# Kernel optimization log

Measured on AMD Instinct MI355X. Metric: run time of the kernel, lower is better.

The kernel has to match this reference:

```python
import jax, jax.numpy as jnp
import numpy as np
import math

D_MODEL = 1024
N_HEADS = 16
D_HEAD = D_MODEL // N_HEADS
DECAY_MAX = 0.99  # buggy torch init: only the LAST head's decay rate survives the loop
LN_EPS = 1e-5


def setup_inputs() -> dict:
    key = jax.random.key(0)
    ks = jax.random.split(key, 12)
    B, S = 2, 2048
    x = jax.random.normal(ks[0], (B, S, D_MODEL), dtype=jnp.float32)
    def w(k):
        return jax.random.normal(k, (D_MODEL, D_MODEL), dtype=jnp.float32) * 0.02
    return {
        "x": x,
        "Wq": w(ks[1]), "bq": jnp.zeros((D_MODEL,), jnp.float32),
        "Wk": w(ks[2]), "bk": jnp.zeros((D_MODEL,), jnp.float32),
        "Wv": w(ks[3]), "bv": jnp.zeros((D_MODEL,), jnp.float32),
        "Wg": w(ks[4]), "bg": jnp.zeros((D_MODEL,), jnp.float32),
        "Wo": w(ks[5]), "bo": jnp.zeros((D_MODEL,), jnp.float32),
        "gamma": jnp.ones((D_MODEL,), jnp.float32),
        "beta": jnp.zeros((D_MODEL,), jnp.float32),
    }


def _decay_mask(S):
    # faithful to torch buffer: decay_matrix[i,j] = DECAY_MAX**(i-j) for j<=i else 0
    i = jnp.arange(S, dtype=jnp.float32)[:, None]
    j = jnp.arange(S, dtype=jnp.float32)[None, :]
    diff = i - j
    return jnp.where(diff >= 0, jnp.power(jnp.float32(DECAY_MAX), diff), 0.0)  # [S,S]


def reference(x, Wq, bq, Wk, bk, Wv, bv, Wg, bg, Wo, bo, gamma, beta):
    B, S, D = x.shape
    H, DH = N_HEADS, D_HEAD
    # projections -> [B,H,S,DH]
    Q = (x @ Wq + bq).reshape(B, S, H, DH).transpose(0, 2, 1, 3)
    K = (x @ Wk + bk).reshape(B, S, H, DH).transpose(0, 2, 1, 3)
    V = (x @ Wv + bv).reshape(B, S, H, DH).transpose(0, 2, 1, 3)
    scores = jnp.einsum('bhsd,bhtd->bhst', Q, K) / math.sqrt(DH)  # [B,H,S,S]
    mask = _decay_mask(S)  # [S,S], broadcast over B,H (head-independent per torch bug)
    retained = jnp.einsum('bhst,bhtd->bhsd', scores * mask, V)
    retained = retained.transpose(0, 2, 1, 3).reshape(B, S, D)
    # LayerNorm over last dim
    mu = jnp.mean(retained, axis=-1, keepdims=True)
    var = jnp.var(retained, axis=-1, keepdims=True)
    normed = (retained - mu) * jax.lax.rsqrt(var + LN_EPS) * gamma + beta
    G = jax.nn.sigmoid(x @ Wg + bg)
    return (normed * G) @ Wo + bo  # dropout = identity (eval)
```

## Files before the change

### kernel.cpp

```cpp
#include <hip/hip_runtime.h>

typedef __attribute__((ext_vector_type(4))) float f32x4;
typedef __attribute__((ext_vector_type(8))) short bf16x8;
typedef unsigned short USHORT;

static __device__ __forceinline__ float bf2f(USHORT u) {
    return __uint_as_float(((unsigned)u) << 16);
}
static __device__ __forceinline__ USHORT f2bf(float f) {
    unsigned u = __float_as_uint(f);
    unsigned r = u + 0x7FFF + ((u >> 16) & 1);
    return (USHORT)(r >> 16);
}

#define GLDS16(gp, lp) __builtin_amdgcn_global_load_lds(                      \
    (const __attribute__((address_space(1))) unsigned int*)(gp),              \
    (__attribute__((address_space(3))) unsigned int*)(lp), 16, 0, 0)

#define FULL_BARRIER() asm volatile("s_waitcnt vmcnt(0) lgkmcnt(0)\ns_barrier" ::: "memory")

#define D64 0.52559648f
#define L2D (-0.014499569695115089f)

struct PrepArgs { const float* src[5]; USHORT* dst[5]; const float* x; USHORT* xb; };

__global__ __launch_bounds__(256) void k_prep(PrepArgs pa) {
    const int z = blockIdx.z;
    const int tid = threadIdx.x;
    __shared__ USHORT t[64][65];
    if (z < 5) {
        const float* __restrict__ W  = pa.src[z];
        USHORT* __restrict__      WT = pa.dst[z];
        const int k0 = blockIdx.y * 64, n0 = blockIdx.x * 64;
#pragma unroll
        for (int s = 0; s < 4; s++) {
            int slot = tid + s * 256;
            int row = slot >> 4, c4 = (slot & 15) * 4;
            float4 vv = *(const float4*)&W[(size_t)(k0 + row) * 1024 + n0 + c4];
            t[row][c4 + 0] = f2bf(vv.x);
            t[row][c4 + 1] = f2bf(vv.y);
            t[row][c4 + 2] = f2bf(vv.z);
            t[row][c4 + 3] = f2bf(vv.w);
        }
        __syncthreads();
#pragma unroll
        for (int s = 0; s < 2; s++) {
            int slot = tid + s * 256;
            int n = slot >> 3, c8 = (slot & 7) * 8;
            USHORT tmp[8];
#pragma unroll
            for (int u = 0; u < 8; u++) tmp[u] = t[c8 + u][n];
            *(int4*)&WT[(size_t)(n0 + n) * 1024 + k0 + c8] = *(int4*)tmp;
        }
    } else {
        const int bi = blockIdx.y * 16 + blockIdx.x;
        const float* xs = pa.x + (size_t)bi * 16384;
        USHORT* xd = pa.xb + (size_t)bi * 16384;
#pragma unroll
        for (int u = 0; u < 16; u++) {
            int idx = u * 1024 + tid * 4;
            float4 v = *(const float4*)&xs[idx];
            *(ushort4*)&xd[idx] = make_ushort4(f2bf(v.x), f2bf(v.y), f2bf(v.z), f2bf(v.w));
        }
    }
}

struct GArgs {
    const USHORT* A;
    const USHORT* W[4];
    const float*  bias[4];
    void*         dst[4];
    USHORT*       dstv;
    float         scale[4];
    int           mode[4];
};

__global__ __launch_bounds__(256, 2) void k_gemm(GArgs ga) {
    const int z = blockIdx.z;
    const USHORT* __restrict__ A  = ga.A;
    const USHORT* __restrict__ BT = ga.W[z];
    __shared__ USHORT As[2][128 * 32];
    __shared__ USHORT Bs[2][128 * 32];
    const int tid = threadIdx.x;
    const int m0 = blockIdx.y * 128, n0 = blockIdx.x * 128;
    const int w = tid >> 6, l = tid & 63, lr = l & 15, q = l >> 4;
    const int wr = w >> 1, wc = w & 1;
    const int srow = tid >> 2, sco = (tid & 3) * 8;
    f32x4 acc[4][4] = {};
    GLDS16(&A [(size_t)(m0 + srow)      * 1024 + sco], &As[0][srow * 32 + sco]);
    GLDS16(&A [(size_t)(m0 + srow + 64) * 1024 + sco], &As[0][(srow + 64) * 32 + sco]);
    GLDS16(&BT[(size_t)(n0 + srow)      * 1024 + sco], &Bs[0][srow * 32 + sco]);
    GLDS16(&BT[(size_t)(n0 + srow + 64) * 1024 + sco], &Bs[0][(srow + 64) * 32 + sco]);
    for (int kt = 0; kt < 32; kt++) {
        const int cur = kt & 1;
        FULL_BARRIER();
        if (kt + 1 < 32) {
            const int k1 = (kt + 1) * 32;
            const int nxt = 1 - cur;
            GLDS16(&A [(size_t)(m0 + srow)      * 1024 + k1 + sco], &As[nxt][srow * 32 + sco]);
            GLDS16(&A [(size_t)(m0 + srow + 64) * 1024 + k1 + sco], &As[nxt][(srow + 64) * 32 + sco]);
            GLDS16(&BT[(size_t)(n0 + srow)      * 1024 + k1 + sco], &Bs[nxt][srow * 32 + sco]);
            GLDS16(&BT[(size_t)(n0 + srow + 64) * 1024 + k1 + sco], &Bs[nxt][(srow + 64) * 32 + sco]);
        }
        bf16x8 af[4], bfr[4];
#pragma unroll
        for (int mi = 0; mi < 4; mi++)
            af[mi] = *(const bf16x8*)&As[cur][(wr * 64 + mi * 16 + lr) * 32 + q * 8];
#pragma unroll
        for (int ni = 0; ni < 4; ni++)
            bfr[ni] = *(const bf16x8*)&Bs[cur][(wc * 64 + ni * 16 + lr) * 32 + q * 8];
#pragma unroll
        for (int mi = 0; mi < 4; mi++)
#pragma unroll
            for (int ni = 0; ni < 4; ni++)
                acc[mi][ni] = __builtin_amdgcn_mfma_f32_16x16x32_bf16(
                    af[mi], bfr[ni], acc[mi][ni], 0, 0, 0);
    }
    const float scale = ga.scale[z];
    const int mode = ga.mode[z];
    const float* __restrict__ bias = ga.bias[z];
#pragma unroll
    for (int ni = 0; ni < 4; ni++) {
        int col = n0 + wc * 64 + ni * 16 + lr;
        float bv = bias[col];
#pragma unroll
        for (int mi = 0; mi < 4; mi++) {
            int r0 = m0 + wr * 64 + mi * 16 + q * 4;
            float vr[4];
#pragma unroll
            for (int r = 0; r < 4; r++) {
                float v = acc[mi][ni][r] + bv;
                if (mode == 1) v = 1.0f / (1.0f + __expf(-v));
                vr[r] = v * scale;
            }
            if (mode == 3) {
                float* df = (float*)ga.dst[z];
#pragma unroll
                for (int r = 0; r < 4; r++)
                    df[(size_t)(r0 + r) * 1024 + col] = vr[r];
            } else if (mode == 2) {
                int b = r0 >> 11, s = r0 & 2047;
                int h = col >> 6, d = col & 63;
                const float NP1 = 1.0101010101010102f;
                float c0 = exp2f(-L2D * (float)(s & 63));
                float c1 = c0 * NP1, c2 = c1 * NP1, c3 = c2 * NP1;
                *(ushort4*)&ga.dstv[(size_t)(((b * 16 + h) * 64) + d) * 2048 + s] =
                    make_ushort4(f2bf(vr[0] * c0), f2bf(vr[1] * c1),
                                 f2bf(vr[2] * c2), f2bf(vr[3] * c3));
            } else {
                USHORT* db = (USHORT*)ga.dst[z];
#pragma unroll
                for (int r = 0; r < 4; r++)
                    db[(size_t)(r0 + r) * 1024 + col] = f2bf(vr[r]);
            }
        }
    }
}

__global__ __launch_bounds__(256) void k_attn_u(const USHORT* __restrict__ K,
                                                const USHORT* __restrict__ VT,
                                                float* __restrict__ U) {
    const int bh = blockIdx.x, c = blockIdx.y;
    const int b = bh >> 4, h = bh & 15;
    const int tid = threadIdx.x, w = tid >> 6, l = tid & 63, lr = l & 15, q = l >> 4;
    __shared__ USHORT KT[64 * 72];
    __shared__ USHORT Vs[64 * 72];
#pragma unroll
    for (int s = 0; s < 2; s++) {
        int slot = tid + s * 256;
        int row = slot >> 3, co = (slot & 7) * 8;
        USHORT kv[8];
        *(int4*)kv = *(const int4*)&K[(size_t)(b * 2048 + c * 64 + row) * 1024 + h * 64 + co];
#pragma unroll
        for (int u = 0; u < 8; u++) KT[(co + u) * 72 + row] = kv[u];
        *(int4*)&Vs[row * 72 + co] =
            *(const int4*)&VT[(size_t)(bh * 64 + row) * 2048 + c * 64 + co];
    }
    __syncthreads();
    f32x4 acc[4] = {};
    bf16x8 av[2];
#pragma unroll
    for (int kk = 0; kk < 2; kk++)
        av[kk] = *(const bf16x8*)&Vs[(w * 16 + lr) * 72 + kk * 32 + q * 8];
#pragma unroll
    for (int dkt = 0; dkt < 4; dkt++)
#pragma unroll
        for (int kk = 0; kk < 2; kk++) {
            bf16x8 bk = *(const bf16x8*)&KT[(dkt * 16 + lr) * 72 + kk * 32 + q * 8];
            acc[dkt] = __builtin_amdgcn_mfma_f32_16x16x32_bf16(av[kk], bk, acc[dkt], 0, 0, 0);
        }
    float* slot = U + (size_t)(bh * 32 + c) * 4096;
#pragma unroll
    for (int dkt = 0; dkt < 4; dkt++)
#pragma unroll
        for (int r = 0; r < 4; r++)
            slot[(w * 16 + q * 4 + r) * 64 + dkt * 16 + lr] = acc[dkt][r] * D64;
}

__global__ __launch_bounds__(256, 2) void k_apply(const USHORT* __restrict__ Q,
                                                  const USHORT* __restrict__ K,
                                                  const USHORT* __restrict__ VT,
                                                  const float* __restrict__ U,
                                                  USHORT* __restrict__ R,
                                                  float* __restrict__ stats) {
    const int bh = blockIdx.x, c = blockIdx.y;
    const int b = bh >> 4, h = bh & 15;
    const int i0 = c * 64;
    const int tid = threadIdx.x, w = tid >> 6, l = tid & 63, lr = l & 15, q = l >> 4;
    __shared__ USHORT Qs[64 * 72];
    __shared__ USHORT Ks[64 * 72];
    __shared__ USHORT Vs[64 * 72];
    __shared__ USHORT Ps[4][16 * 72];
    __shared__ unsigned Spk[4096];
#pragma unroll
    for (int s = 0; s < 2; s++) {
        int slot = tid + s * 256;
        int row = slot >> 3, c8 = (slot & 7) * 8;
        USHORT q8[8];
        *(int4*)q8 = *(const int4*)&Q[(size_t)(b * 2048 + i0 + row) * 1024 + h * 64 + c8];
        const float fr = exp2f(L2D * (float)row);
#pragma unroll
        for (int u = 0; u < 8; u++) q8[u] = f2bf(bf2f(q8[u]) * fr);
        *(int4*)&Qs[row * 72 + c8] = *(int4*)q8;
        *(int4*)&Ks[row * 72 + c8] =
            *(const int4*)&K[(size_t)(b * 2048 + i0 + row) * 1024 + h * 64 + c8];
        *(int4*)&Vs[row * 72 + c8] =
            *(const int4*)&VT[(size_t)(bh * 64 + row) * 2048 + i0 + c8];
    }
    if (c > 0) {
        float sa[16] = {};
        const float* Ub = U + (size_t)bh * 32 * 4096 + tid * 16;
        for (int cp = 0; cp < c; cp++) {
            const float* p = Ub + (size_t)cp * 4096;
#pragma unroll
            for (int u4 = 0; u4 < 4; u4++) {
                float4 uv = *(const float4*)(p + u4 * 4);
                sa[u4 * 4 + 0] = sa[u4 * 4 + 0] * D64 + uv.x;
                sa[u4 * 4 + 1] = sa[u4 * 4 + 1] * D64 + uv.y;
                sa[u4 * 4 + 2] = sa[u4 * 4 + 2] * D64 + uv.z;
                sa[u4 * 4 + 3] = sa[u4 * 4 + 3] * D64 + uv.w;
            }
        }
#pragma unroll
        for (int u = 0; u < 16; u++) {
            USHORT hi = f2bf(sa[u]);
            float  lo = sa[u] - bf2f(hi);
            Spk[tid * 16 + u] = (unsigned)hi | ((unsigned)f2bf(lo) << 16);
        }
    }
    __syncthreads();
    bf16x8 bqf[2];
#pragma unroll
    for (int kk = 0; kk < 2; kk++)
        bqf[kk] = *(const bf16x8*)&Qs[(w * 16 + lr) * 72 + kk * 32 + q * 8];
    f32x4 accr[4] = {};
    if (c > 0) {
#pragma unroll
        for (int dt = 0; dt < 4; dt++)
#pragma unroll
            for (int kk = 0; kk < 2; kk++) {
                const unsigned* sp = &Spk[(dt * 16 + lr) * 64 + kk * 32 + q * 8];
                uint4 pa = *(const uint4*)sp;
                uint4 pb = *(const uint4*)(sp + 4);
                unsigned pk[8] = { pa.x, pa.y, pa.z, pa.w, pb.x, pb.y, pb.z, pb.w };
                bf16x8 hi, lo;
#pragma unroll
                for (int u = 0; u < 8; u++) {
                    hi[u] = (short)(pk[u] & 0xffffu);
                    lo[u] = (short)(pk[u] >> 16);
                }
                accr[dt] = __builtin_amdgcn_mfma_f32_16x16x32_bf16(hi, bqf[kk], accr[dt], 0, 0, 0);
                accr[dt] = __builtin_amdgcn_mfma_f32_16x16x32_bf16(lo, bqf[kk], accr[dt], 0, 0, 0);
            }
    }
    {
        f32x4 accp[4] = {};
#pragma unroll
        for (int kk = 0; kk < 2; kk++)
#pragma unroll
            for (int jt = 0; jt < 4; jt++) {
                bf16x8 akf = *(const bf16x8*)&Ks[(jt * 16 + lr) * 72 + kk * 32 + q * 8];
                accp[jt] = __builtin_amdgcn_mfma_f32_16x16x32_bf16(akf, bqf[kk], accp[jt], 0, 0, 0);
            }
        const int ii = w * 16 + lr;
#pragma unroll
        for (int jt = 0; jt < 4; jt++) {
            const int jj = jt * 16 + q * 4;
            float v0 = (jj + 0 <= ii) ? accp[jt][0] : 0.0f;
            float v1 = (jj + 1 <= ii) ? accp[jt][1] : 0.0f;
            float v2 = (jj + 2 <= ii) ? accp[jt][2] : 0.0f;
            float v3 = (jj + 3 <= ii) ? accp[jt][3] : 0.0f;
            unsigned w0 = __builtin_amdgcn_perm(
                __float_as_uint(v1), __float_as_uint(v0), 0x07060302u);
            unsigned w1 = __builtin_amdgcn_perm(
                __float_as_uint(v3), __float_as_uint(v2), 0x07060302u);
            *(uint2*)&Ps[w][lr * 72 + jt * 16 + q * 4] = make_uint2(w0, w1);
        }
        asm volatile("s_waitcnt lgkmcnt(0)" ::: "memory");
#pragma unroll
        for (int kk = 0; kk < 2; kk++) {
            bf16x8 bpf = *(const bf16x8*)&Ps[w][lr * 72 + kk * 32 + q * 8];
#pragma unroll
            for (int dt = 0; dt < 4; dt++) {
                bf16x8 avf = *(const bf16x8*)&Vs[(dt * 16 + lr) * 72 + kk * 32 + q * 8];
                accr[dt] = __builtin_amdgcn_mfma_f32_16x16x32_bf16(avf, bpf, accr[dt], 0, 0, 0);
            }
        }
    }
    {
        float s1 = 0.f, s2 = 0.f;
#pragma unroll
        for (int dt = 0; dt < 4; dt++)
#pragma unroll
            for (int r = 0; r < 4; r++) {
                float v = accr[dt][r];
                s1 += v; s2 += v * v;
            }
        s1 += __shfl_down(s1, 32); s2 += __shfl_down(s2, 32);
        s1 += __shfl_down(s1, 16); s2 += __shfl_down(s2, 16);
        if (q == 0) {
            int row = b * 2048 + i0 + w * 16 + lr;
            *(float2*)&stats[((size_t)row * 16 + h) * 2] = make_float2(s1, s2);
        }
    }
    {
        const int i = i0 + w * 16 + lr;
#pragma unroll
        for (int dt = 0; dt < 4; dt++) {
            f32x4 a = accr[dt];
            *(ushort4*)&R[(size_t)(b * 2048 + i) * 1024 + h * 64 + dt * 16 + q * 4] =
                make_ushort4(f2bf(a[0]), f2bf(a[1]), f2bf(a[2]), f2bf(a[3]));
        }
    }
}

__global__ __launch_bounds__(256) void k_ln_gate(const USHORT* __restrict__ R,
                                                 const USHORT* __restrict__ G,
                                                 const float* __restrict__ stats,
                                                 const float* __restrict__ gamma,
                                                 const float* __restrict__ beta,
                                                 USHORT* __restrict__ NG) {
    const int row = blockIdx.x, tid = threadIdx.x;
    float s1 = 0.f, s2 = 0.f;
    const float* sp = &stats[(size_t)row * 32];
#pragma unroll
    for (int hh = 0; hh < 8; hh++) {
        float4 v = *(const float4*)(sp + hh * 4);
        s1 += v.x + v.z; s2 += v.y + v.w;
    }
    const float mu  = s1 * (1.0f / 1024.0f);
    const float var = s2 * (1.0f / 1024.0f) - mu * mu;
    const float inv = rsqrtf(fmaxf(var, 0.0f) + 1e-5f);
    ushort4 rv = *(const ushort4*)&R[(size_t)row * 1024 + tid * 4];
    ushort4 g4 = *(const ushort4*)&G[(size_t)row * 1024 + tid * 4];
    float4 gm = *(const float4*)&gamma[tid * 4];
    float4 bt = *(const float4*)&beta[tid * 4];
    float  vv[4]  = { bf2f(rv.x), bf2f(rv.y), bf2f(rv.z), bf2f(rv.w) };
    USHORT gg[4]  = { g4.x, g4.y, g4.z, g4.w };
    float  gmm[4] = { gm.x, gm.y, gm.z, gm.w };
    float  btt[4] = { bt.x, bt.y, bt.z, bt.w };
    USHORT o4[4];
#pragma unroll
    for (int u = 0; u < 4; u++) {
        float nv = (vv[u] - mu) * inv * gmm[u] + btt[u];
        o4[u] = f2bf(nv * bf2f(gg[u]));
    }
    *(ushort4*)&NG[(size_t)row * 1024 + tid * 4] = make_ushort4(o4[0], o4[1], o4[2], o4[3]);
}

extern "C" void kernel_launch(void* const* d_in, const int* in_sizes, int n_in,
                              void* d_out, int out_size, void* d_ws, size_t ws_size,
                              hipStream_t stream) {
    const float* x     = (const float*)d_in[0];
    const float* Wq    = (const float*)d_in[1];
    const float* bq    = (const float*)d_in[2];
    const float* Wk    = (const float*)d_in[3];
    const float* bk    = (const float*)d_in[4];
    const float* Wv    = (const float*)d_in[5];
    const float* bv    = (const float*)d_in[6];
    const float* Wg    = (const float*)d_in[7];
    const float* bg    = (const float*)d_in[8];
    const float* Wo    = (const float*)d_in[9];
    const float* bo    = (const float*)d_in[10];
    const float* gamma = (const float*)d_in[11];
    const float* beta  = (const float*)d_in[12];

    char* ws = (char*)d_ws;
    const size_t MB = 1 << 20;
    USHORT* WqT = (USHORT*)(ws + 0 * MB);
    USHORT* WkT = (USHORT*)(ws + 2 * MB);
    USHORT* WvT = (USHORT*)(ws + 4 * MB);
    USHORT* WgT = (USHORT*)(ws + 6 * MB);
    USHORT* WoT = (USHORT*)(ws + 8 * MB);
    USHORT* Qb  = (USHORT*)(ws + 10 * MB);
    USHORT* Kb  = (USHORT*)(ws + 18 * MB);
    USHORT* VTb = (USHORT*)(ws + 26 * MB);
    USHORT* Gb  = (USHORT*)(ws + 34 * MB);
    float*  Sts = (float*) (ws + 42 * MB);
    USHORT* NGb = Qb;
    USHORT* Xb  = (USHORT*)d_out;
    float*  Ust = (float*)d_out;

    {
        PrepArgs pa;
        pa.src[0] = Wq; pa.src[1] = Wk; pa.src[2] = Wv; pa.src[3] = Wg; pa.src[4] = Wo;
        pa.dst[0] = WqT; pa.dst[1] = WkT; pa.dst[2] = WvT; pa.dst[3] = WgT; pa.dst[4] = WoT;
        pa.x = x; pa.xb = Xb;
        k_prep<<<dim3(16, 16, 6), 256, 0, stream>>>(pa);
    }
    {
        GArgs ga;
        ga.A = Xb;
        ga.W[0] = WqT; ga.W[1] = WkT; ga.W[2] = WvT; ga.W[3] = WgT;
        ga.bias[0] = bq; ga.bias[1] = bk; ga.bias[2] = bv; ga.bias[3] = bg;
        ga.dst[0] = Qb; ga.dst[1] = Kb; ga.dst[2] = nullptr; ga.dst[3] = Gb;
        ga.dstv = VTb;
        ga.scale[0] = 0.125f; ga.scale[1] = 1.0f; ga.scale[2] = 1.0f; ga.scale[3] = 1.0f;
        ga.mode[0] = 0; ga.mode[1] = 0; ga.mode[2] = 2; ga.mode[3] = 1;
        k_gemm<<<dim3(8, 32, 4), 256, 0, stream>>>(ga);
    }
    k_attn_u<<<dim3(32, 32), 256, 0, stream>>>(Kb, VTb, Ust);
    k_apply<<<dim3(32, 32), 256, 0, stream>>>(Qb, Kb, VTb, Ust, Kb, Sts);
    k_ln_gate<<<4096, 256, 0, stream>>>(Kb, Gb, Sts, gamma, beta, NGb);
    {
        GArgs go;
        go.A = NGb;
        for (int i = 0; i < 4; i++) {
            go.W[i] = WoT; go.bias[i] = bo; go.dst[i] = d_out;
            go.scale[i] = 1.0f; go.mode[i] = 3;
        }
        go.dstv = nullptr;
        k_gemm<<<dim3(8, 32, 1), 256, 0, stream>>>(go);
    }
}
```

Before: 217.4 us.

## Fuse chunk-state, apply and LayerNorm-gate into one persistent kernel with grid barriers

Replaces the k_attn_u, k_apply and k_ln_gate launches with a single persistent 256-block kernel that uses software grid barriers between phases. It also replaces the per-chunk O(c) prefix recurrence over U states with a separate parallel scan phase that writes packed hi/lo bf16 prefix states in place, so each apply unit loads one precomputed state. This removes launch gaps and the quadratic prefix-sum reads. The trade-offs are that only 256 blocks of work run, the spin barriers need every block resident at once, and each block handles four units one after another.

```diff
diff --git a/kernel.cpp b/kernel.cpp
--- a/kernel.cpp
+++ b/kernel.cpp
@@ -22,7 +22,20 @@
 #define D64 0.52559648f
 #define L2D (-0.014499569695115089f)
 
-struct PrepArgs { const float* src[5]; USHORT* dst[5]; const float* x; USHORT* xb; };
+static __device__ __forceinline__ void grid_barrier(unsigned* cnt) {
+    __syncthreads();
+    if (threadIdx.x == 0) {
+        __threadfence();
+        atomicAdd(cnt, 1u);
+        while (__hip_atomic_load(cnt, __ATOMIC_RELAXED,
+                                 __HIP_MEMORY_SCOPE_AGENT) < 256u) {}
+        __threadfence();
+    }
+    __syncthreads();
+}
+
+struct PrepArgs { const float* src[5]; USHORT* dst[5]; const float* x; USHORT* xb;
+                  unsigned* bar; };
 
 __global__ __launch_bounds__(256) void k_prep(PrepArgs pa) {
     const int z = blockIdx.z;
@@ -54,6 +67,7 @@
         }
     } else {
         const int bi = blockIdx.y * 16 + blockIdx.x;
+        if (bi == 0 && tid < 8) pa.bar[tid] = 0u;
         const float* xs = pa.x + (size_t)bi * 16384;
         USHORT* xd = pa.xb + (size_t)bi * 16384;
 #pragma unroll
@@ -157,215 +171,222 @@
     }
 }
 
-__global__ __launch_bounds__(256) void k_attn_u(const USHORT* __restrict__ K,
-                                                const USHORT* __restrict__ VT,
-                                                float* __restrict__ U) {
-    const int bh = blockIdx.x, c = blockIdx.y;
-    const int b = bh >> 4, h = bh & 15;
-    const int tid = threadIdx.x, w = tid >> 6, l = tid & 63, lr = l & 15, q = l >> 4;
-    __shared__ USHORT KT[64 * 72];
-    __shared__ USHORT Vs[64 * 72];
-#pragma unroll
-    for (int s = 0; s < 2; s++) {
-        int slot = tid + s * 256;
-        int row = slot >> 3, co = (slot & 7) * 8;
-        USHORT kv[8];
-        *(int4*)kv = *(const int4*)&K[(size_t)(b * 2048 + c * 64 + row) * 1024 + h * 64 + co];
-#pragma unroll
-        for (int u = 0; u < 8; u++) KT[(co + u) * 72 + row] = kv[u];
-        *(int4*)&Vs[row * 72 + co] =
-            *(const int4*)&VT[(size_t)(bh * 64 + row) * 2048 + c * 64 + co];
-    }
-    __syncthreads();
-    f32x4 acc[4] = {};
-    bf16x8 av[2];
-#pragma unroll
-    for (int kk = 0; kk < 2; kk++)
-        av[kk] = *(const bf16x8*)&Vs[(w * 16 + lr) * 72 + kk * 32 + q * 8];
-#pragma unroll
-    for (int dkt = 0; dkt < 4; dkt++)
-#pragma unroll
-        for (int kk = 0; kk < 2; kk++) {
-            bf16x8 bk = *(const bf16x8*)&KT[(dkt * 16 + lr) * 72 + kk * 32 + q * 8];
-            acc[dkt] = __builtin_amdgcn_mfma_f32_16x16x32_bf16(av[kk], bk, acc[dkt], 0, 0, 0);
-        }
-    float* slot = U + (size_t)(bh * 32 + c) * 4096;
-#pragma unroll
-    for (int dkt = 0; dkt < 4; dkt++)
-#pragma unroll
-        for (int r = 0; r < 4; r++)
-            slot[(w * 16 + q * 4 + r) * 64 + dkt * 16 + lr] = acc[dkt][r] * D64;
-}
-
-__global__ __launch_bounds__(256, 2) void k_apply(const USHORT* __restrict__ Q,
-                                                  const USHORT* __restrict__ K,
-                                                  const USHORT* __restrict__ VT,
-                                                  const float* __restrict__ U,
-                                                  USHORT* __restrict__ R,
-                                                  float* __restrict__ stats) {
-    const int bh = blockIdx.x, c = blockIdx.y;
-    const int b = bh >> 4, h = bh & 15;
-    const int i0 = c * 64;
+__global__ __launch_bounds__(256) void k_mega(const USHORT* __restrict__ Q,
+                                              USHORT* __restrict__ KR,
+                                              const USHORT* __restrict__ VT,
+                                              float* __restrict__ Ust,
+                                              float* __restrict__ stats,
+                                              const USHORT* __restrict__ G,
+                                              const float* __restrict__ gamma,
+                                              const float* __restrict__ beta,
+                                              USHORT* __restrict__ NG,
+                                              unsigned* __restrict__ bar) {
     const int tid = threadIdx.x, w = tid >> 6, l = tid & 63, lr = l & 15, q = l >> 4;
     __shared__ USHORT Qs[64 * 72];
     __shared__ USHORT Ks[64 * 72];
     __shared__ USHORT Vs[64 * 72];
     __shared__ USHORT Ps[4][16 * 72];
     __shared__ unsigned Spk[4096];
-#pragma unroll
-    for (int s = 0; s < 2; s++) {
-        int slot = tid + s * 256;
-        int row = slot >> 3, c8 = (slot & 7) * 8;
-        USHORT q8[8];
-        *(int4*)q8 = *(const int4*)&Q[(size_t)(b * 2048 + i0 + row) * 1024 + h * 64 + c8];
-        const float fr = exp2f(L2D * (float)row);
-#pragma unroll
-        for (int u = 0; u < 8; u++) q8[u] = f2bf(bf2f(q8[u]) * fr);
-        *(int4*)&Qs[row * 72 + c8] = *(int4*)q8;
-        *(int4*)&Ks[row * 72 + c8] =
-            *(const int4*)&K[(size_t)(b * 2048 + i0 + row) * 1024 + h * 64 + c8];
-        *(int4*)&Vs[row * 72 + c8] =
-            *(const int4*)&VT[(size_t)(bh * 64 + row) * 2048 + i0 + c8];
-    }
-    if (c > 0) {
-        float sa[16] = {};
-        const float* Ub = U + (size_t)bh * 32 * 4096 + tid * 16;
-        for (int cp = 0; cp < c; cp++) {
-            const float* p = Ub + (size_t)cp * 4096;
-#pragma unroll
-            for (int u4 = 0; u4 < 4; u4++) {
-                float4 uv = *(const float4*)(p + u4 * 4);
-                sa[u4 * 4 + 0] = sa[u4 * 4 + 0] * D64 + uv.x;
-                sa[u4 * 4 + 1] = sa[u4 * 4 + 1] * D64 + uv.y;
-                sa[u4 * 4 + 2] = sa[u4 * 4 + 2] * D64 + uv.z;
-                sa[u4 * 4 + 3] = sa[u4 * 4 + 3] * D64 + uv.w;
-            }
-        }
-#pragma unroll
-        for (int u = 0; u < 16; u++) {
-            USHORT hi = f2bf(sa[u]);
-            float  lo = sa[u] - bf2f(hi);
-            Spk[tid * 16 + u] = (unsigned)hi | ((unsigned)f2bf(lo) << 16);
-        }
-    }
-    __syncthreads();
-    bf16x8 bqf[2];
-#pragma unroll
-    for (int kk = 0; kk < 2; kk++)
-        bqf[kk] = *(const bf16x8*)&Qs[(w * 16 + lr) * 72 + kk * 32 + q * 8];
-    f32x4 accr[4] = {};
-    if (c > 0) {
-#pragma unroll
-        for (int dt = 0; dt < 4; dt++)
+    for (int u0 = 0; u0 < 4; u0++) {
+        const int unit = blockIdx.x * 4 + u0;
+        const int bh = unit >> 5, c = unit & 31;
+        const int b = bh >> 4, h = bh & 15;
+        USHORT* KT = Qs;
+        __syncthreads();
+#pragma unroll
+        for (int s = 0; s < 2; s++) {
+            int slot = tid + s * 256;
+            int row = slot >> 3, co = (slot & 7) * 8;
+            USHORT kv[8];
+            *(int4*)kv = *(const int4*)&KR[(size_t)(b * 2048 + c * 64 + row) * 1024 + h * 64 + co];
+#pragma unroll
+            for (int uu = 0; uu < 8; uu++) KT[(co + uu) * 72 + row] = kv[uu];
+            *(int4*)&Vs[row * 72 + co] =
+                *(const int4*)&VT[(size_t)(bh * 64 + row) * 2048 + c * 64 + co];
+        }
+        __syncthreads();
+        f32x4 acc[4] = {};
+        bf16x8 av[2];
+#pragma unroll
+        for (int kk = 0; kk < 2; kk++)
+            av[kk] = *(const bf16x8*)&Vs[(w * 16 + lr) * 72 + kk * 32 + q * 8];
+#pragma unroll
+        for (int dkt = 0; dkt < 4; dkt++)
 #pragma unroll
             for (int kk = 0; kk < 2; kk++) {
-                const unsigned* sp = &Spk[(dt * 16 + lr) * 64 + kk * 32 + q * 8];
-                uint4 pa = *(const uint4*)sp;
-                uint4 pb = *(const uint4*)(sp + 4);
-                unsigned pk[8] = { pa.x, pa.y, pa.z, pa.w, pb.x, pb.y, pb.z, pb.w };
-                bf16x8 hi, lo;
-#pragma unroll
-                for (int u = 0; u < 8; u++) {
-                    hi[u] = (short)(pk[u] & 0xffffu);
-                    lo[u] = (short)(pk[u] >> 16);
+                bf16x8 bk = *(const bf16x8*)&KT[(dkt * 16 + lr) * 72 + kk * 32 + q * 8];
+                acc[dkt] = __builtin_amdgcn_mfma_f32_16x16x32_bf16(av[kk], bk, acc[dkt], 0, 0, 0);
+            }
+        float* slot = Ust + (size_t)(bh * 32 + c) * 4096;
+#pragma unroll
+        for (int dkt = 0; dkt < 4; dkt++)
+#pragma unroll
+            for (int r = 0; r < 4; r++)
+                slot[(w * 16 + q * 4 + r) * 64 + dkt * 16 + lr] = acc[dkt][r] * D64;
+    }
+    grid_barrier(&bar[0]);
+    if (blockIdx.x < 128) {
+        const int bh = blockIdx.x >> 2, dvg = blockIdx.x & 3;
+        const int dv = dvg * 16 + (tid >> 4), dk4 = (tid & 15) * 4;
+        float s0 = 0.f, s1 = 0.f, s2 = 0.f, s3 = 0.f;
+        for (int c = 0; c < 32; c++) {
+            float* p = Ust + (size_t)(bh * 32 + c) * 4096 + dv * 64 + dk4;
+            float4 uv = *(const float4*)p;
+            s0 = s0 * D64 + uv.x; s1 = s1 * D64 + uv.y;
+            s2 = s2 * D64 + uv.z; s3 = s3 * D64 + uv.w;
+            unsigned pk[4];
+            float sv[4] = { s0, s1, s2, s3 };
+#pragma unroll
+            for (int r = 0; r < 4; r++) {
+                USHORT hi = f2bf(sv[r]);
+                float  lo = sv[r] - bf2f(hi);
+                pk[r] = (unsigned)hi | ((unsigned)f2bf(lo) << 16);
+            }
+            *(uint4*)p = make_uint4(pk[0], pk[1], pk[2], pk[3]);
+        }
+    }
+    grid_barrier(&bar[1]);
+    for (int u0 = 0; u0 < 4; u0++) {
+        const int unit = blockIdx.x * 4 + u0;
+        const int bh = unit >> 5, c = unit & 31;
+        const int b = bh >> 4, h = bh & 15;
+        const int i0 = c * 64;
+        __syncthreads();
+#pragma unroll
+        for (int s = 0; s < 2; s++) {
+            int slot = tid + s * 256;
+            int row = slot >> 3, c8 = (slot & 7) * 8;
+            USHORT q8[8];
+            *(int4*)q8 = *(const int4*)&Q[(size_t)(b * 2048 + i0 + row) * 1024 + h * 64 + c8];
+            const float fr = exp2f(L2D * (float)row);
+#pragma unroll
+            for (int uu = 0; uu < 8; uu++) q8[uu] = f2bf(bf2f(q8[uu]) * fr);
+            *(int4*)&Qs[row * 72 + c8] = *(int4*)q8;
+            *(int4*)&Ks[row * 72 + c8] =
+                *(const int4*)&KR[(size_t)(b * 2048 + i0 + row) * 1024 + h * 64 + c8];
+            *(int4*)&Vs[row * 72 + c8] =
+                *(const int4*)&VT[(size_t)(bh * 64 + row) * 2048 + i0 + c8];
+        }
+        if (c > 0) {
+            const uint4* sg = (const uint4*)(Ust + (size_t)(bh * 32 + c - 1) * 4096);
+#pragma unroll
+            for (int s = 0; s < 4; s++)
+                ((uint4*)Spk)[tid + s * 256] = sg[tid + s * 256];
+        }
+        __syncthreads();
+        bf16x8 bqf[2];
+#pragma unroll
+        for (int kk = 0; kk < 2; kk++)
+            bqf[kk] = *(const bf16x8*)&Qs[(w * 16 + lr) * 72 + kk * 32 + q * 8];
+        f32x4 accr[4] = {};
+        if (c > 0) {
+#pragma unroll
+            for (int dt = 0; dt < 4; dt++)
+#pragma unroll
+                for (int kk = 0; kk < 2; kk++) {
+                    const unsigned* sp = &Spk[(dt * 16 + lr) * 64 + kk * 32 + q * 8];
+                    uint4 pa = *(const uint4*)sp;
+                    uint4 pb = *(const uint4*)(sp + 4);
+                    unsigned pk[8] = { pa.x, pa.y, pa.z, pa.w, pb.x, pb.y, pb.z, pb.w };
+                    bf16x8 hi, lo;
+#pragma unroll
+                    for (int uu = 0; uu < 8; uu++) {
+                        hi[uu] = (short)(pk[uu] & 0xffffu);
+                        lo[uu] = (short)(pk[uu] >> 16);
+                    }
+                    accr[dt] = __builtin_amdgcn_mfma_f32_16x16x32_bf16(hi, bqf[kk], accr[dt], 0, 0, 0);
+                    accr[dt] = __builtin_amdgcn_mfma_f32_16x16x32_bf16(lo, bqf[kk], accr[dt], 0, 0, 0);
                 }
-                accr[dt] = __builtin_amdgcn_mfma_f32_16x16x32_bf16(hi, bqf[kk], accr[dt], 0, 0, 0);
-                accr[dt] = __builtin_amdgcn_mfma_f32_16x16x32_bf16(lo, bqf[kk], accr[dt], 0, 0, 0);
-            }
-    }
-    {
-        f32x4 accp[4] = {};
-#pragma unroll
-        for (int kk = 0; kk < 2; kk++)
+        }
+        {
+            f32x4 accp[4] = {};
+#pragma unroll
+            for (int kk = 0; kk < 2; kk++)
+#pragma unroll
+                for (int jt = 0; jt < 4; jt++) {
+                    bf16x8 akf = *(const bf16x8*)&Ks[(jt * 16 + lr) * 72 + kk * 32 + q * 8];
+                    accp[jt] = __builtin_amdgcn_mfma_f32_16x16x32_bf16(akf, bqf[kk], accp[jt], 0, 0, 0);
+                }
+            const int ii = w * 16 + lr;
 #pragma unroll
             for (int jt = 0; jt < 4; jt++) {
-                bf16x8 akf = *(const bf16x8*)&Ks[(jt * 16 + lr) * 72 + kk * 32 + q * 8];
-                accp[jt] = __builtin_amdgcn_mfma_f32_16x16x32_bf16(akf, bqf[kk], accp[jt], 0, 0, 0);
-            }
-        const int ii = w * 16 + lr;
-#pragma unroll
-        for (int jt = 0; jt < 4; jt++) {
-            const int jj = jt * 16 + q * 4;
-            float v0 = (jj + 0 <= ii) ? accp[jt][0] : 0.0f;
-            float v1 = (jj + 1 <= ii) ? accp[jt][1] : 0.0f;
-            float v2 = (jj + 2 <= ii) ? accp[jt][2] : 0.0f;
-            float v3 = (jj + 3 <= ii) ? accp[jt][3] : 0.0f;
-            unsigned w0 = __builtin_amdgcn_perm(
-                __float_as_uint(v1), __float_as_uint(v0), 0x07060302u);
-            unsigned w1 = __builtin_amdgcn_perm(
-                __float_as_uint(v3), __float_as_uint(v2), 0x07060302u);
-            *(uint2*)&Ps[w][lr * 72 + jt * 16 + q * 4] = make_uint2(w0, w1);
-        }
-        asm volatile("s_waitcnt lgkmcnt(0)" ::: "memory");
-#pragma unroll
-        for (int kk = 0; kk < 2; kk++) {
-            bf16x8 bpf = *(const bf16x8*)&Ps[w][lr * 72 + kk * 32 + q * 8];
+                const int jj = jt * 16 + q * 4;
+                float v0 = (jj + 0 <= ii) ? accp[jt][0] : 0.0f;
+                float v1 = (jj + 1 <= ii) ? accp[jt][1] : 0.0f;
+                float v2 = (jj + 2 <= ii) ? accp[jt][2] : 0.0f;
+                float v3 = (jj + 3 <= ii) ? accp[jt][3] : 0.0f;
+                unsigned w0 = __builtin_amdgcn_perm(
+                    __float_as_uint(v1), __float_as_uint(v0), 0x07060302u);
+                unsigned w1 = __builtin_amdgcn_perm(
+                    __float_as_uint(v3), __float_as_uint(v2), 0x07060302u);
+                *(uint2*)&Ps[w][lr * 72 + jt * 16 + q * 4] = make_uint2(w0, w1);
+            }
+            asm volatile("s_waitcnt lgkmcnt(0)" ::: "memory");
+#pragma unroll
+            for (int kk = 0; kk < 2; kk++) {
+                bf16x8 bpf = *(const bf16x8*)&Ps[w][lr * 72 + kk * 32 + q * 8];
+#pragma unroll
+                for (int dt = 0; dt < 4; dt++) {
+                    bf16x8 avf = *(const bf16x8*)&Vs[(dt * 16 + lr) * 72 + kk * 32 + q * 8];
+                    accr[dt] = __builtin_amdgcn_mfma_f32_16x16x32_bf16(avf, bpf, accr[dt], 0, 0, 0);
+                }
+            }
+        }
+        {
+            float s1 = 0.f, s2 = 0.f;
+#pragma unroll
+            for (int dt = 0; dt < 4; dt++)
+#pragma unroll
+                for (int r = 0; r < 4; r++) {
+                    float v = accr[dt][r];
+                    s1 += v; s2 += v * v;
+                }
+            s1 += __shfl_down(s1, 32); s2 += __shfl_down(s2, 32);
+            s1 += __shfl_down(s1, 16); s2 += __shfl_down(s2, 16);
+            if (q == 0) {
+                int row = b * 2048 + i0 + w * 16 + lr;
+                *(float2*)&stats[((size_t)row * 16 + h) * 2] = make_float2(s1, s2);
+            }
+        }
+        {
+            const int i = i0 + w * 16 + lr;
 #pragma unroll
             for (int dt = 0; dt < 4; dt++) {
-                bf16x8 avf = *(const bf16x8*)&Vs[(dt * 16 + lr) * 72 + kk * 32 + q * 8];
-                accr[dt] = __builtin_amdgcn_mfma_f32_16x16x32_bf16(avf, bpf, accr[dt], 0, 0, 0);
-            }
-        }
-    }
-    {
+                f32x4 a = accr[dt];
+                *(ushort4*)&KR[(size_t)(b * 2048 + i) * 1024 + h * 64 + dt * 16 + q * 4] =
+                    make_ushort4(f2bf(a[0]), f2bf(a[1]), f2bf(a[2]), f2bf(a[3]));
+            }
+        }
+    }
+    grid_barrier(&bar[2]);
+    for (int rr = 0; rr < 16; rr++) {
+        const int row = blockIdx.x * 16 + rr;
         float s1 = 0.f, s2 = 0.f;
-#pragma unroll
-        for (int dt = 0; dt < 4; dt++)
-#pragma unroll
-            for (int r = 0; r < 4; r++) {
-                float v = accr[dt][r];
-                s1 += v; s2 += v * v;
-            }
-        s1 += __shfl_down(s1, 32); s2 += __shfl_down(s2, 32);
-        s1 += __shfl_down(s1, 16); s2 += __shfl_down(s2, 16);
-        if (q == 0) {
-            int row = b * 2048 + i0 + w * 16 + lr;
-            *(float2*)&stats[((size_t)row * 16 + h) * 2] = make_float2(s1, s2);
-        }
-    }
-    {
-        const int i = i0 + w * 16 + lr;
-#pragma unroll
-        for (int dt = 0; dt < 4; dt++) {
-            f32x4 a = accr[dt];
-            *(ushort4*)&R[(size_t)(b * 2048 + i) * 1024 + h * 64 + dt * 16 + q * 4] =
-                make_ushort4(f2bf(a[0]), f2bf(a[1]), f2bf(a[2]), f2bf(a[3]));
-        }
-    }
-}
-
-__global__ __launch_bounds__(256) void k_ln_gate(const USHORT* __restrict__ R,
-                                                 const USHORT* __restrict__ G,
-                                                 const float* __restrict__ stats,
-                                                 const float* __restrict__ gamma,
-                                                 const float* __restrict__ beta,
-                                                 USHORT* __restrict__ NG) {
-    const int row = blockIdx.x, tid = threadIdx.x;
-    float s1 = 0.f, s2 = 0.f;
-    const float* sp = &stats[(size_t)row * 32];
-#pragma unroll
-    for (int hh = 0; hh < 8; hh++) {
-        float4 v = *(const float4*)(sp + hh * 4);
-        s1 += v.x + v.z; s2 += v.y + v.w;
-    }
-    const float mu  = s1 * (1.0f / 1024.0f);
-    const float var = s2 * (1.0f / 1024.0f) - mu * mu;
-    const float inv = rsqrtf(fmaxf(var, 0.0f) + 1e-5f);
-    ushort4 rv = *(const ushort4*)&R[(size_t)row * 1024 + tid * 4];
-    ushort4 g4 = *(const ushort4*)&G[(size_t)row * 1024 + tid * 4];
-    float4 gm = *(const float4*)&gamma[tid * 4];
-    float4 bt = *(const float4*)&beta[tid * 4];
-    float  vv[4]  = { bf2f(rv.x), bf2f(rv.y), bf2f(rv.z), bf2f(rv.w) };
-    USHORT gg[4]  = { g4.x, g4.y, g4.z, g4.w };
-    float  gmm[4] = { gm.x, gm.y, gm.z, gm.w };
-    float  btt[4] = { bt.x, bt.y, bt.z, bt.w };
-    USHORT o4[4];
-#pragma unroll
-    for (int u = 0; u < 4; u++) {
-        float nv = (vv[u] - mu) * inv * gmm[u] + btt[u];
-        o4[u] = f2bf(nv * bf2f(gg[u]));
-    }
-    *(ushort4*)&NG[(size_t)row * 1024 + tid * 4] = make_ushort4(o4[0], o4[1], o4[2], o4[3]);
+        const float* sp = &stats[(size_t)row * 32];
+#pragma unroll
+        for (int hh = 0; hh < 8; hh++) {
+            float4 v = *(const float4*)(sp + hh * 4);
+            s1 += v.x + v.z; s2 += v.y + v.w;
+        }
+        const float mu  = s1 * (1.0f / 1024.0f);
+        const float var = s2 * (1.0f / 1024.0f) - mu * mu;
+        const float inv = rsqrtf(fmaxf(var, 0.0f) + 1e-5f);
+        ushort4 rv = *(const ushort4*)&KR[(size_t)row * 1024 + tid * 4];
+        ushort4 g4 = *(const ushort4*)&G[(size_t)row * 1024 + tid * 4];
+        float4 gm = *(const float4*)&gamma[tid * 4];
+        float4 bt = *(const float4*)&beta[tid * 4];
+        float  vv[4]  = { bf2f(rv.x), bf2f(rv.y), bf2f(rv.z), bf2f(rv.w) };
+        USHORT gg[4]  = { g4.x, g4.y, g4.z, g4.w };
+        float  gmm[4] = { gm.x, gm.y, gm.z, gm.w };
+        float  btt[4] = { bt.x, bt.y, bt.z, bt.w };
+        USHORT o4[4];
+#pragma unroll
+        for (int u = 0; u < 4; u++) {
+            float nv = (vv[u] - mu) * inv * gmm[u] + btt[u];
+            o4[u] = f2bf(nv * bf2f(gg[u]));
+        }
+        *(ushort4*)&NG[(size_t)row * 1024 + tid * 4] = make_ushort4(o4[0], o4[1], o4[2], o4[3]);
+    }
 }
 
 extern "C" void kernel_launch(void* const* d_in, const int* in_sizes, int n_in,
@@ -397,6 +418,7 @@
     USHORT* VTb = (USHORT*)(ws + 26 * MB);
     USHORT* Gb  = (USHORT*)(ws + 34 * MB);
     float*  Sts = (float*) (ws + 42 * MB);
+    unsigned* Bar = (unsigned*)(ws + 42 * MB + 512 * 1024);
     USHORT* NGb = Qb;
     USHORT* Xb  = (USHORT*)d_out;
     float*  Ust = (float*)d_out;
@@ -405,7 +427,7 @@
         PrepArgs pa;
         pa.src[0] = Wq; pa.src[1] = Wk; pa.src[2] = Wv; pa.src[3] = Wg; pa.src[4] = Wo;
         pa.dst[0] = WqT; pa.dst[1] = WkT; pa.dst[2] = WvT; pa.dst[3] = WgT; pa.dst[4] = WoT;
-        pa.x = x; pa.xb = Xb;
+        pa.x = x; pa.xb = Xb; pa.bar = Bar;
         k_prep<<<dim3(16, 16, 6), 256, 0, stream>>>(pa);
     }
     {
@@ -419,9 +441,7 @@
         ga.mode[0] = 0; ga.mode[1] = 0; ga.mode[2] = 2; ga.mode[3] = 1;
         k_gemm<<<dim3(8, 32, 4), 256, 0, stream>>>(ga);
     }
-    k_attn_u<<<dim3(32, 32), 256, 0, stream>>>(Kb, VTb, Ust);
-    k_apply<<<dim3(32, 32), 256, 0, stream>>>(Qb, Kb, VTb, Ust, Kb, Sts);
-    k_ln_gate<<<4096, 256, 0, stream>>>(Kb, Gb, Sts, gamma, beta, NGb);
+    k_mega<<<256, 256, 0, stream>>>(Qb, Kb, VTb, Ust, Sts, Gb, gamma, beta, NGb, Bar);
     {
         GArgs go;
         go.A = NGb;
```

Measured after the change: 289.8 us. +33.3%, slower.
